# Kernel tuning notes

Hardware: AMD Instinct MI355X
Metric: run time of the kernel (lower is better)

The kernel has to match this reference:

```python
import jax, jax.numpy as jnp
import numpy as np

N = 100000       # nodes
E = 1600000      # edges (avg degree 16)
F_IN = 128
F_HID = 64
F_OUT = 40
K = 10
ALPHA = 0.1


def setup_inputs() -> dict:
    key = jax.random.key(0)
    k1, k2, k3, k4, k5, k6 = jax.random.split(key, 6)
    x = jax.random.normal(k1, (N, F_IN), dtype=jnp.float32)
    edge_index = jax.random.randint(k2, (2, E), 0, N, dtype=jnp.int32)
    # Linear params (Kaiming-uniform-ish scale)
    W1 = jax.random.normal(k3, (F_IN, F_HID), dtype=jnp.float32) / np.sqrt(F_IN)
    b1 = jax.random.normal(k4, (F_HID,), dtype=jnp.float32) * 0.01
    W2 = jax.random.normal(k5, (F_HID, F_OUT), dtype=jnp.float32) / np.sqrt(F_HID)
    b2 = jax.random.normal(k6, (F_OUT,), dtype=jnp.float32) * 0.01
    return {"x": x, "edge_index": edge_index, "W1": W1, "b1": b1, "W2": W2, "b2": b2}


def _gcn_norm(edge_index, dtype):
    # add self loops, symmetric normalization D^{-1/2} (A+I) D^{-1/2}
    loops = jnp.arange(N, dtype=edge_index.dtype)
    src = jnp.concatenate([edge_index[0], loops])
    dst = jnp.concatenate([edge_index[1], loops])
    deg = jax.ops.segment_sum(jnp.ones_like(src, dtype=dtype), dst, num_segments=N)
    dinv = jnp.where(deg > 0, jax.lax.rsqrt(deg), 0.0).astype(dtype)
    norm = dinv[src] * dinv[dst]  # [E + N]
    return src, dst, norm


def _appnp(x, src, dst, norm):
    h = x  # teleport target
    def step(xc, _):
        agg = jax.ops.segment_sum(xc[src] * norm[:, None], dst, num_segments=N)
        return (1.0 - ALPHA) * agg + ALPHA * h, None
    out, _ = jax.lax.scan(step, x, None, length=K)
    return out


def reference(x, edge_index, W1, b1, W2, b2):
    src, dst, norm = _gcn_norm(edge_index, x.dtype)
    # layer 1: Linear -> relu -> (dropout p=0) -> APPNP
    h = jax.nn.relu(x @ W1 + b1)
    h = _appnp(h, src, dst, norm)
    # layer 2: Linear -> relu -> APPNP
    h = jax.nn.relu(h @ W2 + b2)
    h = _appnp(h, src, dst, norm)
    return jax.nn.log_softmax(h, axis=1)
```

## Files before the change

kernel.cpp:

```cpp
#include <hip/hip_runtime.h>
#include <hip/hip_fp16.h>
#include <hip/hip_fp8.h>

namespace {
constexpr int NN = 100000;
constexpr int NE = 1600000;
constexpr int FIN = 128, FHID = 64, FOUT = 40;
constexpr float ALPHA = 0.1f;
constexpr int SLOTS = 64;

typedef int v4i __attribute__((ext_vector_type(4)));
typedef unsigned int v2u __attribute__((ext_vector_type(2)));
typedef unsigned int v4u __attribute__((ext_vector_type(4)));
typedef float v2f __attribute__((ext_vector_type(2)));
typedef float v4f __attribute__((ext_vector_type(4)));

#if __has_builtin(__builtin_amdgcn_cvt_pk_f32_fp8) && __has_builtin(__builtin_amdgcn_cvt_pk_fp8_f32)
#define HW_FP8 1
#else
#define HW_FP8 0
#endif

__device__ __forceinline__ ushort f2h(float v) {
  union { __half h; ushort u; } cv;
  cv.h = __float2half_rn(v);
  return cv.u;
}

__device__ __forceinline__ void acc8_fp8(v2u w, float* a) {
#if HW_FP8
  v2f p0 = __builtin_amdgcn_cvt_pk_f32_fp8((int)w.x, false);
  v2f p1 = __builtin_amdgcn_cvt_pk_f32_fp8((int)w.x, true);
  v2f p2 = __builtin_amdgcn_cvt_pk_f32_fp8((int)w.y, false);
  v2f p3 = __builtin_amdgcn_cvt_pk_f32_fp8((int)w.y, true);
  a[0] += p0.x; a[1] += p0.y; a[2] += p1.x; a[3] += p1.y;
  a[4] += p2.x; a[5] += p2.y; a[6] += p3.x; a[7] += p3.y;
#else
  union { v2u w; unsigned char b[8]; } cv;
  cv.w = w;
#pragma unroll
  for (int k = 0; k < 8; k++) {
    __hip_fp8_e4m3 h;
    h.__x = cv.b[k];
    a[k] += (float)h;
  }
#endif
}

__device__ __forceinline__ v2u enc8_fp8(const float* o) {
#if HW_FP8
  int d0 = __builtin_amdgcn_cvt_pk_fp8_f32(o[0], o[1], 0, false);
  d0 = __builtin_amdgcn_cvt_pk_fp8_f32(o[2], o[3], d0, true);
  int d1 = __builtin_amdgcn_cvt_pk_fp8_f32(o[4], o[5], 0, false);
  d1 = __builtin_amdgcn_cvt_pk_fp8_f32(o[6], o[7], d1, true);
  v2u r;
  r.x = (unsigned int)d0;
  r.y = (unsigned int)d1;
  return r;
#else
  union { v2u w; unsigned char b[8]; } cv;
#pragma unroll
  for (int k = 0; k < 8; k++) {
    __hip_fp8_e4m3 h(o[k]);
    cv.b[k] = h.__x;
  }
  return cv.w;
#endif
}

__device__ __forceinline__ unsigned char enc1_fp8(float v) {
#if HW_FP8
  return (unsigned char)(__builtin_amdgcn_cvt_pk_fp8_f32(v, v, 0, false) & 0xff);
#else
  __hip_fp8_e4m3 h(v);
  return h.__x;
#endif
}

__global__ void k_zero(int* cnt) {
  int i = blockIdx.x * 256 + threadIdx.x;
  if (i < NN) cnt[i] = 0;
}

__global__ void k_fill_ell(const int* __restrict__ src, const int* __restrict__ dst,
                           int* __restrict__ cnt, int* __restrict__ ell) {
  int e = blockIdx.x * 256 + threadIdx.x;
  if (e >= NE) return;
  int s = src[e], d = dst[e];
  int p = atomicAdd(&cnt[d], 1);
  if (p < SLOTS) ell[(d << 6) + p] = s;
}

__global__ void k_dinv(const int* __restrict__ cnt, float2* __restrict__ dd) {
  int i = blockIdx.x * 256 + threadIdx.x;
  if (i < NN) {
    float di = rsqrtf((float)(cnt[i] + 1));
    dd[i] = make_float2(di, 0.9f * di * di);
  }
}

__global__ __launch_bounds__(256) void k_mlp(const float* __restrict__ x,
                                             const float* __restrict__ W1,
                                             const float* __restrict__ b1,
                                             const float* __restrict__ W2,
                                             const float2* __restrict__ dd,
                                             float* __restrict__ h2x,
                                             ushort* __restrict__ u0,
                                             unsigned char* __restrict__ uq) {
  __shared__ float w1s[FIN * FHID];
  __shared__ float w2s[FHID * FOUT];
  __shared__ float hs[16][FHID];
  for (int i = threadIdx.x; i < FIN * FHID / 4; i += 256)
    ((float4*)w1s)[i] = ((const float4*)W1)[i];
  for (int i = threadIdx.x; i < FHID * FOUT / 4; i += 256)
    ((float4*)w2s)[i] = ((const float4*)W2)[i];
  __syncthreads();
  int ln = threadIdx.x >> 4;
  int ch = threadIdx.x & 15;
  int node = blockIdx.x * 16 + ln;
  const float* xr = x + (size_t)node * FIN;
  float4 acc = {0, 0, 0, 0};
  for (int k = 0; k < FIN; k += 4) {
    float4 xv = *(const float4*)(xr + k);
    float4 w0 = ((const float4*)(w1s + (k + 0) * FHID))[ch];
    float4 w1 = ((const float4*)(w1s + (k + 1) * FHID))[ch];
    float4 w2 = ((const float4*)(w1s + (k + 2) * FHID))[ch];
    float4 w3 = ((const float4*)(w1s + (k + 3) * FHID))[ch];
    acc.x += xv.x * w0.x + xv.y * w1.x + xv.z * w2.x + xv.w * w3.x;
    acc.y += xv.x * w0.y + xv.y * w1.y + xv.z * w2.y + xv.w * w3.y;
    acc.z += xv.x * w0.z + xv.y * w1.z + xv.z * w2.z + xv.w * w3.z;
    acc.w += xv.x * w0.w + xv.y * w1.w + xv.z * w2.w + xv.w * w3.w;
  }
  float4 bb = ((const float4*)b1)[ch];
  hs[ln][ch * 4 + 0] = fmaxf(acc.x + bb.x, 0.f);
  hs[ln][ch * 4 + 1] = fmaxf(acc.y + bb.y, 0.f);
  hs[ln][ch * 4 + 2] = fmaxf(acc.z + bb.z, 0.f);
  hs[ln][ch * 4 + 3] = fmaxf(acc.w + bb.w, 0.f);
  __syncthreads();
  for (int o = threadIdx.x; o < 16 * FOUT; o += 256) {
    int nd = o / FOUT;
    int c = o - nd * FOUT;
    float a = 0.f;
#pragma unroll
    for (int k = 0; k < FHID; k++) a += hs[nd][k] * w2s[k * FOUT + c];
    int gn = blockIdx.x * 16 + nd;
    float u = dd[gn].x * a;
    h2x[(size_t)gn * FOUT + c] = a;
    u0[(size_t)gn * FOUT + c] = f2h(u);
    uq[((size_t)gn << 6) + c] = enc1_fp8(u);
  }
}

__device__ __forceinline__ void gather_ell(const int* __restrict__ ell,
                                           const unsigned char* __restrict__ u,
                                           int node, int ch, int deg, float* a) {
#pragma unroll
  for (int k = 0; k < 8; k++) a[k] = 0.f;
  const unsigned char* ub = u + ch * 8;
  const v4i* ip = (const v4i*)ell + ((size_t)node << 4);
  v2u ws = *(const v2u*)(ub + ((size_t)node << 6));
  v4i q0 = ip[0];
  v4i q1 = ip[1];
  acc8_fp8(ws, a);
  int j = 0;
  for (; j + 8 <= deg; j += 8) {
    int g = (j >> 2) + 2;
    v4i n0 = ip[g > 15 ? 15 : g];
    v4i n1 = ip[g + 1 > 15 ? 15 : g + 1];
    v2u w0 = *(const v2u*)(ub + ((size_t)q0.x << 6));
    v2u w1 = *(const v2u*)(ub + ((size_t)q0.y << 6));
    v2u w2 = *(const v2u*)(ub + ((size_t)q0.z << 6));
    v2u w3 = *(const v2u*)(ub + ((size_t)q0.w << 6));
    v2u w4 = *(const v2u*)(ub + ((size_t)q1.x << 6));
    v2u w5 = *(const v2u*)(ub + ((size_t)q1.y << 6));
    v2u w6 = *(const v2u*)(ub + ((size_t)q1.z << 6));
    v2u w7 = *(const v2u*)(ub + ((size_t)q1.w << 6));
    acc8_fp8(w0, a);
    acc8_fp8(w1, a);
    acc8_fp8(w2, a);
    acc8_fp8(w3, a);
    acc8_fp8(w4, a);
    acc8_fp8(w5, a);
    acc8_fp8(w6, a);
    acc8_fp8(w7, a);
    q0 = n0;
    q1 = n1;
  }
  if (j + 4 <= deg) {
    v2u w0 = *(const v2u*)(ub + ((size_t)q0.x << 6));
    v2u w1 = *(const v2u*)(ub + ((size_t)q0.y << 6));
    v2u w2 = *(const v2u*)(ub + ((size_t)q0.z << 6));
    v2u w3 = *(const v2u*)(ub + ((size_t)q0.w << 6));
    acc8_fp8(w0, a);
    acc8_fp8(w1, a);
    acc8_fp8(w2, a);
    acc8_fp8(w3, a);
    q0 = q1;
    j += 4;
  }
  if (j < deg) {
    int rr = deg - j;
    acc8_fp8(*(const v2u*)(ub + ((size_t)q0.x << 6)), a);
    if (rr > 1) acc8_fp8(*(const v2u*)(ub + ((size_t)q0.y << 6)), a);
    if (rr > 2) acc8_fp8(*(const v2u*)(ub + ((size_t)q0.z << 6)), a);
  }
}

#define APPNP_HDR(cntp)                            \
  int tid = threadIdx.x;                           \
  int nd = tid / 5, ch = tid - nd * 5;             \
  int node = blockIdx.x * 64 + nd;                 \
  if (node >= NN) return;                          \
  int deg = (cntp)[node];                          \
  deg = deg > SLOTS ? SLOTS : deg;

__device__ __forceinline__ void store_h8(ushort* p, const float* v) {
  union { v4u u; __half h[8]; } cv;
#pragma unroll
  for (int k = 0; k < 8; k++) cv.h[k] = __float2half_rn(v[k]);
  *(v4u*)p = cv.u;
}

__global__ __launch_bounds__(320, 6) void k_mid(const int* __restrict__ cnt,
                                                const int* __restrict__ ell,
                                                const float2* __restrict__ dd,
                                                const ushort* __restrict__ u0,
                                                const unsigned char* __restrict__ u,
                                                unsigned char* __restrict__ un) {
  APPNP_HDR(cnt)
  union { v4u q; __half h[8]; } t0;
  t0.q = *(const v4u*)(u0 + (size_t)node * FOUT + ch * 8);
  float c9 = dd[node].y;
  float a[8];
  gather_ell(ell, u, node, ch, deg, a);
  float o[8];
#pragma unroll
  for (int k = 0; k < 8; k++) o[k] = c9 * a[k] + ALPHA * __half2float(t0.h[k]);
  v2u st = enc8_fp8(o);
  *(v2u*)(un + ((size_t)node << 6) + ch * 8) = st;
}

__global__ __launch_bounds__(320, 6) void k_final1(const int* __restrict__ cnt,
                                                   const int* __restrict__ ell,
                                                   const float2* __restrict__ dd,
                                                   const float* __restrict__ b2,
                                                   const float* __restrict__ h2x,
                                                   const unsigned char* __restrict__ u,
                                                   ushort* __restrict__ gh,
                                                   ushort* __restrict__ u0n,
                                                   unsigned char* __restrict__ uqn) {
  APPNP_HDR(cnt)
  float di = dd[node].x;
  v4f h0 = __builtin_nontemporal_load((const v4f*)(h2x + (size_t)node * FOUT + ch * 8));
  v4f h1 = __builtin_nontemporal_load((const v4f*)(h2x + (size_t)node * FOUT + ch * 8 + 4));
  const float* bb = b2 + ch * 8;
  float a[8];
  gather_ell(ell, u, node, ch, deg, a);
  float t9 = 0.9f * di;
  float hx[8] = {h0.x, h0.y, h0.z, h0.w, h1.x, h1.y, h1.z, h1.w};
  float g[8], ug[8];
#pragma unroll
  for (int k = 0; k < 8; k++) {
    float z = t9 * a[k] + ALPHA * hx[k] + bb[k];
    g[k] = fmaxf(z, 0.f);
    ug[k] = di * g[k];
  }
  store_h8(gh + (size_t)node * FOUT + ch * 8, g);
  store_h8(u0n + (size_t)node * FOUT + ch * 8, ug);
  v2u st = enc8_fp8(ug);
  *(v2u*)(uqn + ((size_t)node << 6) + ch * 8) = st;
}

__global__ __launch_bounds__(320, 6) void k_final2(const int* __restrict__ cnt,
                                                   const int* __restrict__ ell,
                                                   const float2* __restrict__ dd,
                                                   const ushort* __restrict__ gh,
                                                   const unsigned char* __restrict__ u,
                                                   ushort* __restrict__ zh) {
  APPNP_HDR(cnt)
  union { v4u q; __half h[8]; } hv;
  hv.q = *(const v4u*)(gh + (size_t)node * FOUT + ch * 8);
  float t9 = 0.9f * dd[node].x;
  float a[8];
  gather_ell(ell, u, node, ch, deg, a);
  float o[8];
#pragma unroll
  for (int k = 0; k < 8; k++) o[k] = t9 * a[k] + ALPHA * __half2float(hv.h[k]);
  store_h8(zh + (size_t)node * FOUT + ch * 8, o);
}

__global__ void k_logsoftmax(const ushort* __restrict__ in, float* __restrict__ out) {
  int i = blockIdx.x * 256 + threadIdx.x;
  if (i >= NN) return;
  union { v4u q; __half h[8]; } v[5];
  const v4u* r = (const v4u*)(in + (size_t)i * FOUT);
  float f[40];
  float m = -1e30f;
#pragma unroll
  for (int j = 0; j < 5; j++) {
    v[j].q = r[j];
#pragma unroll
    for (int k = 0; k < 8; k++) {
      f[j * 8 + k] = __half2float(v[j].h[k]);
      m = fmaxf(m, f[j * 8 + k]);
    }
  }
  float sum = 0.f;
#pragma unroll
  for (int j = 0; j < 40; j++) sum += expf(f[j] - m);
  float lse = m + logf(sum);
  float4* o = (float4*)(out + (size_t)i * FOUT);
#pragma unroll
  for (int j = 0; j < 10; j++) {
    float4 w = {f[j * 4] - lse, f[j * 4 + 1] - lse, f[j * 4 + 2] - lse, f[j * 4 + 3] - lse};
    o[j] = w;
  }
}

}

extern "C" void kernel_launch(void* const* d_in, const int* in_sizes, int n_in,
                              void* d_out, int out_size, void* d_ws, size_t ws_size,
                              hipStream_t stream) {
  const float* x = (const float*)d_in[0];
  const int* ei = (const int*)d_in[1];
  const int* src = ei;
  const int* dst = ei + NE;
  const float* W1 = (const float*)d_in[2];
  const float* b1 = (const float*)d_in[3];
  const float* W2 = (const float*)d_in[4];
  const float* b2 = (const float*)d_in[5];
  float* out = (float*)d_out;

  char* ws = (char*)d_ws;
  size_t off = 0;
  auto alloc = [&](size_t bytes) -> void* {
    void* p = ws + off;
    off += (bytes + 255) & ~(size_t)255;
    return p;
  };
  int* cnt          = (int*)alloc((size_t)NN * 4);
  float2* dd        = (float2*)alloc((size_t)NN * 8);
  int* ell          = (int*)alloc((size_t)NN * SLOTS * 4);
  float* h2x        = (float*)alloc((size_t)NN * FOUT * 4);
  ushort* u0h       = (ushort*)alloc((size_t)NN * FOUT * 2);
  ushort* gh        = (ushort*)alloc((size_t)NN * FOUT * 2);
  ushort* zh        = (ushort*)alloc((size_t)NN * FOUT * 2);
  unsigned char* q0 = (unsigned char*)alloc((size_t)NN * 64);
  unsigned char* qA = (unsigned char*)alloc((size_t)NN * 64);
  unsigned char* qB = (unsigned char*)alloc((size_t)NN * 64);

  k_zero<<<(NN + 255) / 256, 256, 0, stream>>>(cnt);
  k_fill_ell<<<NE / 256, 256, 0, stream>>>(src, dst, cnt, ell);
  k_dinv<<<(NN + 255) / 256, 256, 0, stream>>>(cnt, dd);

  k_mlp<<<NN / 16, 256, 0, stream>>>(x, W1, b1, W2, dd, h2x, u0h, q0);

  int agrid = (NN + 63) / 64;
  const unsigned char* cu = q0;
  for (int it = 0; it < 9; it++) {
    unsigned char* nx = (it & 1) ? qB : qA;
    k_mid<<<agrid, 320, 0, stream>>>(cnt, ell, dd, u0h, cu, nx);
    cu = nx;
  }
  k_final1<<<agrid, 320, 0, stream>>>(cnt, ell, dd, b2, h2x, cu, gh, u0h, q0);

  cu = q0;
  for (int it = 0; it < 9; it++) {
    unsigned char* nx = (it & 1) ? qB : qA;
    k_mid<<<agrid, 320, 0, stream>>>(cnt, ell, dd, u0h, cu, nx);
    cu = nx;
  }
  k_final2<<<agrid, 320, 0, stream>>>(cnt, ell, dd, gh, cu, zh);

  k_logsoftmax<<<(NN + 255) / 256, 256, 0, stream>>>(zh, out);
}
```

Measured before the change: 788.9 us.

## Pack fp8 node features at 40-byte stride and chunk ELL fill launches

Shrinks the per-node fp8 feature row from a 64-byte stride to a 40-byte stride, so the gathered table is smaller and fits better in cache and uses less bandwidth during the APPNP gathers. It also splits the ELL fill into eight sequential launches of 200k edges each, which changes the order in which edges claim slots and may reduce atomic contention or improve write locality. The cost is that rows are no longer aligned to 64 bytes, so an 8-byte gather can straddle cache lines, and the extra launches add overhead.

```diff
diff --git a/kernel.cpp b/kernel.cpp
--- a/kernel.cpp
+++ b/kernel.cpp
@@ -8,6 +8,8 @@
 constexpr int FIN = 128, FHID = 64, FOUT = 40;
 constexpr float ALPHA = 0.1f;
 constexpr int SLOTS = 64;
+constexpr int SB = 40;
+constexpr int ECHUNK = 200000;
 
 typedef int v4i __attribute__((ext_vector_type(4)));
 typedef unsigned int v2u __attribute__((ext_vector_type(2)));
@@ -83,9 +85,9 @@
 }
 
 __global__ void k_fill_ell(const int* __restrict__ src, const int* __restrict__ dst,
-                           int* __restrict__ cnt, int* __restrict__ ell) {
-  int e = blockIdx.x * 256 + threadIdx.x;
-  if (e >= NE) return;
+                           int* __restrict__ cnt, int* __restrict__ ell, int ebase) {
+  int e = ebase + blockIdx.x * 256 + threadIdx.x;
+  if (e >= ebase + ECHUNK || e >= NE) return;
   int s = src[e], d = dst[e];
   int p = atomicAdd(&cnt[d], 1);
   if (p < SLOTS) ell[(d << 6) + p] = s;
@@ -147,7 +149,7 @@
     float u = dd[gn].x * a;
     h2x[(size_t)gn * FOUT + c] = a;
     u0[(size_t)gn * FOUT + c] = f2h(u);
-    uq[((size_t)gn << 6) + c] = enc1_fp8(u);
+    uq[(size_t)gn * SB + c] = enc1_fp8(u);
   }
 }
 
@@ -158,7 +160,7 @@
   for (int k = 0; k < 8; k++) a[k] = 0.f;
   const unsigned char* ub = u + ch * 8;
   const v4i* ip = (const v4i*)ell + ((size_t)node << 4);
-  v2u ws = *(const v2u*)(ub + ((size_t)node << 6));
+  v2u ws = *(const v2u*)(ub + (size_t)node * SB);
   v4i q0 = ip[0];
   v4i q1 = ip[1];
   acc8_fp8(ws, a);
@@ -167,14 +169,14 @@
     int g = (j >> 2) + 2;
     v4i n0 = ip[g > 15 ? 15 : g];
     v4i n1 = ip[g + 1 > 15 ? 15 : g + 1];
-    v2u w0 = *(const v2u*)(ub + ((size_t)q0.x << 6));
-    v2u w1 = *(const v2u*)(ub + ((size_t)q0.y << 6));
-    v2u w2 = *(const v2u*)(ub + ((size_t)q0.z << 6));
-    v2u w3 = *(const v2u*)(ub + ((size_t)q0.w << 6));
-    v2u w4 = *(const v2u*)(ub + ((size_t)q1.x << 6));
-    v2u w5 = *(const v2u*)(ub + ((size_t)q1.y << 6));
-    v2u w6 = *(const v2u*)(ub + ((size_t)q1.z << 6));
-    v2u w7 = *(const v2u*)(ub + ((size_t)q1.w << 6));
+    v2u w0 = *(const v2u*)(ub + (size_t)q0.x * SB);
+    v2u w1 = *(const v2u*)(ub + (size_t)q0.y * SB);
+    v2u w2 = *(const v2u*)(ub + (size_t)q0.z * SB);
+    v2u w3 = *(const v2u*)(ub + (size_t)q0.w * SB);
+    v2u w4 = *(const v2u*)(ub + (size_t)q1.x * SB);
+    v2u w5 = *(const v2u*)(ub + (size_t)q1.y * SB);
+    v2u w6 = *(const v2u*)(ub + (size_t)q1.z * SB);
+    v2u w7 = *(const v2u*)(ub + (size_t)q1.w * SB);
     acc8_fp8(w0, a);
     acc8_fp8(w1, a);
     acc8_fp8(w2, a);
@@ -187,10 +189,10 @@
     q1 = n1;
   }
   if (j + 4 <= deg) {
-    v2u w0 = *(const v2u*)(ub + ((size_t)q0.x << 6));
-    v2u w1 = *(const v2u*)(ub + ((size_t)q0.y << 6));
-    v2u w2 = *(const v2u*)(ub + ((size_t)q0.z << 6));
-    v2u w3 = *(const v2u*)(ub + ((size_t)q0.w << 6));
+    v2u w0 = *(const v2u*)(ub + (size_t)q0.x * SB);
+    v2u w1 = *(const v2u*)(ub + (size_t)q0.y * SB);
+    v2u w2 = *(const v2u*)(ub + (size_t)q0.z * SB);
+    v2u w3 = *(const v2u*)(ub + (size_t)q0.w * SB);
     acc8_fp8(w0, a);
     acc8_fp8(w1, a);
     acc8_fp8(w2, a);
@@ -200,9 +202,9 @@
   }
   if (j < deg) {
     int rr = deg - j;
-    acc8_fp8(*(const v2u*)(ub + ((size_t)q0.x << 6)), a);
-    if (rr > 1) acc8_fp8(*(const v2u*)(ub + ((size_t)q0.y << 6)), a);
-    if (rr > 2) acc8_fp8(*(const v2u*)(ub + ((size_t)q0.z << 6)), a);
+    acc8_fp8(*(const v2u*)(ub + (size_t)q0.x * SB), a);
+    if (rr > 1) acc8_fp8(*(const v2u*)(ub + (size_t)q0.y * SB), a);
+    if (rr > 2) acc8_fp8(*(const v2u*)(ub + (size_t)q0.z * SB), a);
   }
 }
 
@@ -237,7 +239,7 @@
 #pragma unroll
   for (int k = 0; k < 8; k++) o[k] = c9 * a[k] + ALPHA * __half2float(t0.h[k]);
   v2u st = enc8_fp8(o);
-  *(v2u*)(un + ((size_t)node << 6) + ch * 8) = st;
+  *(v2u*)(un + (size_t)node * SB + ch * 8) = st;
 }
 
 __global__ __launch_bounds__(320, 6) void k_final1(const int* __restrict__ cnt,
@@ -268,7 +270,7 @@
   store_h8(gh + (size_t)node * FOUT + ch * 8, g);
   store_h8(u0n + (size_t)node * FOUT + ch * 8, ug);
   v2u st = enc8_fp8(ug);
-  *(v2u*)(uqn + ((size_t)node << 6) + ch * 8) = st;
+  *(v2u*)(uqn + (size_t)node * SB + ch * 8) = st;
 }
 
 __global__ __launch_bounds__(320, 6) void k_final2(const int* __restrict__ cnt,
@@ -346,12 +348,13 @@
   ushort* u0h       = (ushort*)alloc((size_t)NN * FOUT * 2);
   ushort* gh        = (ushort*)alloc((size_t)NN * FOUT * 2);
   ushort* zh        = (ushort*)alloc((size_t)NN * FOUT * 2);
-  unsigned char* q0 = (unsigned char*)alloc((size_t)NN * 64);
-  unsigned char* qA = (unsigned char*)alloc((size_t)NN * 64);
-  unsigned char* qB = (unsigned char*)alloc((size_t)NN * 64);
+  unsigned char* q0 = (unsigned char*)alloc((size_t)NN * SB);
+  unsigned char* qA = (unsigned char*)alloc((size_t)NN * SB);
+  unsigned char* qB = (unsigned char*)alloc((size_t)NN * SB);
 
   k_zero<<<(NN + 255) / 256, 256, 0, stream>>>(cnt);
-  k_fill_ell<<<NE / 256, 256, 0, stream>>>(src, dst, cnt, ell);
+  for (int c = 0; c < NE / ECHUNK; c++)
+    k_fill_ell<<<(ECHUNK + 255) / 256, 256, 0, stream>>>(src, dst, cnt, ell, c * ECHUNK);
   k_dinv<<<(NN + 255) / 256, 256, 0, stream>>>(cnt, dd);
 
   k_mlp<<<NN / 16, 256, 0, stream>>>(x, W1, b1, W2, dd, h2x, u0h, q0);
```

Measured after the change: 706.3 us. 10.5% less time.
